# Optimization experiments

Measured on AMD Instinct MI355X. Metric: run time of the kernel, lower is better.

The kernel has to match this reference:

```python
import jax, jax.numpy as jnp
import numpy as np

B, P, D, H, DH = 2, 2048, 1024, 16, 64
EPS = 1e-5

def layernorm(x, g, b):
    mu = jnp.mean(x, axis=-1, keepdims=True)
    var = jnp.mean((x - mu) ** 2, axis=-1, keepdims=True)
    return (x - mu) * jax.lax.rsqrt(var + EPS) * g + b

def setup_inputs() -> dict:
    key = jax.random.key(0)
    ks = jax.random.split(key, 16)
    s = lambda *sh: 1.0 / np.sqrt(sh[-2] if len(sh) > 1 else sh[-1])
    return {
        "x": jax.random.normal(ks[0], (B, P, D), jnp.float32),
        "Wq": jax.random.normal(ks[1], (H, D, DH), jnp.float32) / np.sqrt(D),
        "Wk": jax.random.normal(ks[2], (H, D, DH), jnp.float32) / np.sqrt(D),
        "Wv": jax.random.normal(ks[3], (H, D, DH), jnp.float32) / np.sqrt(D),
        "Wp": jax.random.normal(ks[4], (D, D), jnp.float32) / np.sqrt(D),
        "bp": jax.random.normal(ks[5], (D,), jnp.float32) * 0.01,
        "W1": jax.random.normal(ks[6], (D, 4 * D), jnp.float32) / np.sqrt(D),
        "b1": jax.random.normal(ks[7], (4 * D,), jnp.float32) * 0.01,
        "W2": jax.random.normal(ks[8], (4 * D, D), jnp.float32) / np.sqrt(4 * D),
        "b2": jax.random.normal(ks[9], (D,), jnp.float32) * 0.01,
        "g1": jnp.ones((D,), jnp.float32),
        "be1": jnp.zeros((D,), jnp.float32),
        "g2": jnp.ones((D,), jnp.float32),
        "be2": jnp.zeros((D,), jnp.float32),
    }

def reference(x, Wq, Wk, Wv, Wp, bp, W1, b1, W2, b2, g1, be1, g2, be2):
    Bb, Pp, Dd = x.shape
    h = layernorm(x, g1, be1)
    # per-head projections, stacked: [B,H,P,DH]
    q = jnp.einsum('bpd,hde->bhpe', h, Wq)
    k = jnp.einsum('bpd,hde->bhpe', h, Wk)
    v = jnp.einsum('bpd,hde->bhpe', h, Wv)
    # NOTE: source scales by dim_embd**-0.5 (C = x.shape[-1]), not dim_head
    scores = jnp.einsum('bhpe,bhqe->bhpq', q, k) * (Dd ** -0.5)
    mask = jnp.tril(jnp.ones((Pp, Pp), bool))
    scores = jnp.where(mask, scores, -jnp.inf)
    att = jax.nn.softmax(scores, axis=-1)
    o = jnp.einsum('bhpq,bhqe->bhpe', att, v)
    # concat heads: [B,P,H*DH]
    o = o.transpose(0, 2, 1, 3).reshape(Bb, Pp, -1)
    x = x + o @ Wp + bp
    h2 = layernorm(x, g2, be2)
    m = jax.nn.gelu(h2 @ W1 + b1, approximate=False)
    x = x + m @ W2 + b2
    return x
```

## Files before the change

kernel.cpp:

```cpp
#include <hip/hip_runtime.h>
#include <hip/hip_bf16.h>
#include <stdint.h>

typedef unsigned short u16;
typedef __attribute__((ext_vector_type(4))) float f32x4;
typedef __attribute__((ext_vector_type(8))) short bf16x8;
typedef __attribute__((ext_vector_type(4))) short bf16x4;
typedef __attribute__((ext_vector_type(4))) unsigned short u16x4;

static __device__ __forceinline__ u16 f2bf(float f) {
    union { float f; unsigned u; } v; v.f = f;
    unsigned r = v.u + 0x7fffu + ((v.u >> 16) & 1u);
    return (u16)(r >> 16);
}

static __device__ __forceinline__ void gload_lds16(const u16* g, u16* l) {
    __builtin_amdgcn_global_load_lds(
        (const __attribute__((address_space(1))) void*)(uintptr_t)g,
        (__attribute__((address_space(3))) void*)(uint32_t)(uintptr_t)l,
        16, 0, 0);
}

__global__ __launch_bounds__(256) void transpose_cast_b(
    const float* __restrict__ W, u16* __restrict__ out,
    int K, int N, long in_bs, long out_bs)
{
    __shared__ float tile[32][33];
    const float* Wb = W + (size_t)blockIdx.z * in_bs;
    u16* ob = out + (size_t)blockIdx.z * out_bs;
    int nt = blockIdx.x * 32, kt = blockIdx.y * 32;
    int tx = threadIdx.x & 31, ty = threadIdx.x >> 5;
    #pragma unroll
    for (int i = ty; i < 32; i += 8)
        tile[i][tx] = Wb[(size_t)(kt + i) * N + nt + tx];
    __syncthreads();
    #pragma unroll
    for (int i = ty; i < 32; i += 8)
        ob[(size_t)(nt + i) * K + kt + tx] = f2bf(tile[tx][i]);
}

__global__ __launch_bounds__(256) void ln_kernel(
    const float* __restrict__ x, const float* __restrict__ g,
    const float* __restrict__ be, u16* __restrict__ out)
{
    int row = blockIdx.x;
    int t = threadIdx.x;
    const float4* xr = (const float4*)(x + (size_t)row * 1024);
    float4 v = xr[t];
    float s = v.x + v.y + v.z + v.w;
    float sq = v.x * v.x + v.y * v.y + v.z * v.z + v.w * v.w;
    #pragma unroll
    for (int o = 1; o < 64; o <<= 1) {
        s  += __shfl_xor(s, o);
        sq += __shfl_xor(sq, o);
    }
    __shared__ float ps[4], pq[4];
    if ((t & 63) == 0) { ps[t >> 6] = s; pq[t >> 6] = sq; }
    __syncthreads();
    float S = ps[0] + ps[1] + ps[2] + ps[3];
    float Q = pq[0] + pq[1] + pq[2] + pq[3];
    float mu = S * (1.0f / 1024.0f);
    float var = Q * (1.0f / 1024.0f) - mu * mu;
    float rs = rsqrtf(var + 1e-5f);
    const float4 g4  = ((const float4*)g)[t];
    const float4 be4 = ((const float4*)be)[t];
    u16x4 o4;
    o4[0] = f2bf((v.x - mu) * rs * g4.x + be4.x);
    o4[1] = f2bf((v.y - mu) * rs * g4.y + be4.y);
    o4[2] = f2bf((v.z - mu) * rs * g4.z + be4.z);
    o4[3] = f2bf((v.w - mu) * rs * g4.w + be4.w);
    *(u16x4*)(out + (size_t)row * 1024 + t * 4) = o4;
}

template<int EPI>
__global__ __launch_bounds__(256) void gemm_bt(
    const u16* __restrict__ A, const u16* __restrict__ Bt,
    int M, int N, int K,
    const float* __restrict__ bias,
    void* __restrict__ Cout, u16* __restrict__ Kf, u16* __restrict__ Vf)
{
    __shared__ __align__(16) u16 SH[32768];
    const int tm = blockIdx.y * 128, tn = blockIdx.x * 128;
    const int t = threadIdx.x;
    const int lane = t & 63, wave = t >> 6;
    const int wr = wave >> 1, wc = wave & 1;
    const int lq = lane & 15, lg = lane >> 4;
    f32x4 acc[4][4] = {};

    const int srow8 = lane >> 3;
    const int skoff = ((lane & 7) ^ srow8) * 8;
    const u16* ag = A  + (size_t)(tm + wave * 32 + srow8) * K + skoff;
    const u16* bg = Bt + (size_t)(tn + wave * 32 + srow8) * K + skoff;

    auto STAGE = [&](int buf, int k0) {
        u16* ab = SH + buf * 16384 + wave * 2048;
        u16* bb = SH + buf * 16384 + 8192 + wave * 2048;
        #pragma unroll
        for (int j = 0; j < 4; ++j) {
            gload_lds16(ag + (size_t)(j * 8) * K + k0, ab + j * 512);
            gload_lds16(bg + (size_t)(j * 8) * K + k0, bb + j * 512);
        }
    };

    const int KT = K >> 6;
    STAGE(0, 0);
    STAGE(1, 64);
    asm volatile("s_waitcnt vmcnt(8)" ::: "memory");
    __builtin_amdgcn_sched_barrier(0);
    __builtin_amdgcn_s_barrier();

    for (int kt = 0; kt < KT; ++kt) {
        const int buf = kt & 1;
        const u16* abuf = SH + buf * 16384;
        const u16* bbuf = abuf + 8192;
        bf16x8 af[4][2], bfv[4][2];
        #pragma unroll
        for (int m = 0; m < 4; ++m) {
            const int row = wr * 64 + m * 16 + lq;
            #pragma unroll
            for (int kk = 0; kk < 2; ++kk) {
                const int slot = (kk * 4 + lg) ^ (row & 7);
                af[m][kk] = *(const bf16x8*)(abuf + row * 64 + slot * 8);
            }
        }
        #pragma unroll
        for (int n = 0; n < 4; ++n) {
            const int col = wc * 64 + n * 16 + lq;
            #pragma unroll
            for (int kk = 0; kk < 2; ++kk) {
                const int slot = (kk * 4 + lg) ^ (col & 7);
                bfv[n][kk] = *(const bf16x8*)(bbuf + col * 64 + slot * 8);
            }
        }
        asm volatile("s_waitcnt lgkmcnt(0)" ::: "memory");
        __builtin_amdgcn_sched_barrier(0);
        __builtin_amdgcn_s_barrier();

        const bool pre = (kt + 2 < KT);
        if (pre) STAGE(buf, (kt + 2) << 6);

        __builtin_amdgcn_s_setprio(1);
        #pragma unroll
        for (int m = 0; m < 4; ++m)
            #pragma unroll
            for (int n = 0; n < 4; ++n)
                #pragma unroll
                for (int kk = 0; kk < 2; ++kk)
                    acc[m][n] = __builtin_amdgcn_mfma_f32_16x16x32_bf16(
                        af[m][kk], bfv[n][kk], acc[m][n], 0, 0, 0);
        __builtin_amdgcn_s_setprio(0);

        if (kt + 1 < KT) {
            if (pre) asm volatile("s_waitcnt vmcnt(8)" ::: "memory");
            else     asm volatile("s_waitcnt vmcnt(0)" ::: "memory");
            __builtin_amdgcn_sched_barrier(0);
            __builtin_amdgcn_s_barrier();
        }
    }

    if (EPI == 2 || (EPI == 3 && tn < 1024)) {
        __syncthreads();
        #pragma unroll
        for (int n = 0; n < 4; ++n) {
            const int cl = wc * 64 + n * 16 + lq;
            #pragma unroll
            for (int m = 0; m < 4; ++m) {
                const int rl = wr * 64 + m * 16 + lg * 4;
                #pragma unroll
                for (int r = 0; r < 4; ++r) {
                    float v = acc[m][n][r];
                    if (EPI == 2) {
                        float xx = v + bias[tn + cl];
                        v = 0.5f * xx * (1.0f + erff(xx * 0.70710678118654752f));
                    }
                    SH[(rl + r) * 136 + cl] = f2bf(v);
                }
            }
        }
        __syncthreads();
        const int row = t >> 1, half = t & 1;
        const int ncols = (EPI == 2) ? N : 1024;
        const uint4* srow4 = (const uint4*)(SH + row * 136 + half * 64);
        uint4* drow = (uint4*)((u16*)Cout + (size_t)(tm + row) * ncols + tn + half * 64);
        #pragma unroll
        for (int i = 0; i < 8; ++i)
            drow[i] = srow4[i];
    } else if (EPI == 3) {
        __syncthreads();
        const bool isK = (tn < 2048);
        #pragma unroll
        for (int n = 0; n < 4; ++n) {
            const int cl = wc * 64 + n * 16 + lq;
            const int d = cl & 63, hl = cl >> 6;
            #pragma unroll
            for (int m = 0; m < 4; ++m) {
                const int rl0 = wr * 64 + m * 16 + lg * 4;
                #pragma unroll
                for (int r = 0; r < 4; ++r) {
                    const int rl = rl0 + r;
                    const int p = rl & 63, kl = rl >> 6;
                    int off;
                    if (isK)
                        off = ((p >> 4) * 2 + (d >> 5)) * 512 + ((d >> 3) & 3) * 128
                            + (p & 15) * 8 + (d & 7);
                    else
                        off = ((p >> 4) * 4 + (d >> 4)) * 256 + ((p >> 2) & 3) * 64
                            + (d & 15) * 4 + (p & 3);
                    SH[(hl * 2 + kl) * 4096 + off] = f2bf(acc[m][n][r]);
                }
            }
        }
        __syncthreads();
        const int img = t >> 6, ln = t & 63;
        const int hl = img >> 1, kl = img & 1;
        const int hh = ((tn - (isK ? 1024 : 2048)) >> 6) + hl;
        const int bb = tm >> 11, pp = tm & 2047;
        u16* base = (isK ? Kf : Vf) + (size_t)(bb * 16 + hh) * 131072
                  + (size_t)((pp >> 6) + kl) * 4096;
        const u16* simg = SH + img * 4096;
        #pragma unroll
        for (int i = 0; i < 8; ++i)
            *(uint4*)(base + ln * 8 + i * 512) = *(const uint4*)(simg + ln * 8 + i * 512);
    }
}

__global__ __launch_bounds__(256) void gemm_bt64(
    const u16* __restrict__ A, const u16* __restrict__ Bt,
    int M, int N, int K,
    const float* __restrict__ bias, const float* __restrict__ res,
    float* __restrict__ Cout)
{
    __shared__ __align__(16) u16 SH[24576];
    const int tm = blockIdx.y * 128, tn = blockIdx.x * 64;
    const int t = threadIdx.x;
    const int lane = t & 63, wave = t >> 6;
    const int wr = wave >> 1, wc = wave & 1;
    const int lq = lane & 15, lg = lane >> 4;
    f32x4 acc[4][2] = {};

    const int srow8 = lane >> 3;
    const int skoff = ((lane & 7) ^ srow8) * 8;
    const u16* ag = A  + (size_t)(tm + wave * 32 + srow8) * K + skoff;
    const u16* bg = Bt + (size_t)(tn + wave * 16 + srow8) * K + skoff;

    auto STAGE = [&](int buf, int k0) {
        u16* ab = SH + buf * 12288 + wave * 2048;
        u16* bb = SH + buf * 12288 + 8192 + wave * 1024;
        #pragma unroll
        for (int j = 0; j < 4; ++j)
            gload_lds16(ag + (size_t)(j * 8) * K + k0, ab + j * 512);
        #pragma unroll
        for (int j = 0; j < 2; ++j)
            gload_lds16(bg + (size_t)(j * 8) * K + k0, bb + j * 512);
    };

    const int KT = K >> 6;
    STAGE(0, 0);
    STAGE(1, 64);
    asm volatile("s_waitcnt vmcnt(6)" ::: "memory");
    __builtin_amdgcn_sched_barrier(0);
    __builtin_amdgcn_s_barrier();

    for (int kt = 0; kt < KT; ++kt) {
        const int buf = kt & 1;
        const u16* abuf = SH + buf * 12288;
        const u16* bbuf = abuf + 8192;
        bf16x8 af[4][2], bfr[2][2];
        #pragma unroll
        for (int m = 0; m < 4; ++m) {
            const int row = wr * 64 + m * 16 + lq;
            #pragma unroll
            for (int kk = 0; kk < 2; ++kk) {
                const int slot = (kk * 4 + lg) ^ (row & 7);
                af[m][kk] = *(const bf16x8*)(abuf + row * 64 + slot * 8);
            }
        }
        #pragma unroll
        for (int n = 0; n < 2; ++n) {
            const int col = wc * 32 + n * 16 + lq;
            #pragma unroll
            for (int kk = 0; kk < 2; ++kk) {
                const int slot = (kk * 4 + lg) ^ (col & 7);
                bfr[n][kk] = *(const bf16x8*)(bbuf + col * 64 + slot * 8);
            }
        }
        asm volatile("s_waitcnt lgkmcnt(0)" ::: "memory");
        __builtin_amdgcn_sched_barrier(0);
        __builtin_amdgcn_s_barrier();

        const bool pre = (kt + 2 < KT);
        if (pre) STAGE(buf, (kt + 2) << 6);

        __builtin_amdgcn_s_setprio(1);
        #pragma unroll
        for (int m = 0; m < 4; ++m)
            #pragma unroll
            for (int n = 0; n < 2; ++n)
                #pragma unroll
                for (int kk = 0; kk < 2; ++kk)
                    acc[m][n] = __builtin_amdgcn_mfma_f32_16x16x32_bf16(
                        af[m][kk], bfr[n][kk], acc[m][n], 0, 0, 0);
        __builtin_amdgcn_s_setprio(0);

        if (kt + 1 < KT) {
            if (pre) asm volatile("s_waitcnt vmcnt(6)" ::: "memory");
            else     asm volatile("s_waitcnt vmcnt(0)" ::: "memory");
            __builtin_amdgcn_sched_barrier(0);
            __builtin_amdgcn_s_barrier();
        }
    }

    #pragma unroll
    for (int m = 0; m < 4; ++m)
        #pragma unroll
        for (int n = 0; n < 2; ++n) {
            const int col = tn + wc * 32 + n * 16 + lq;
            #pragma unroll
            for (int r = 0; r < 4; ++r) {
                const int row = tm + wr * 64 + m * 16 + lg * 4 + r;
                Cout[(size_t)row * N + col] = acc[m][n][r] + bias[col] + res[(size_t)row * N + col];
            }
        }
}

__global__ __launch_bounds__(256, 4) void attn_kernel(
    const u16* __restrict__ qb, const u16* __restrict__ Kf,
    const u16* __restrict__ Vf, u16* __restrict__ o)
{
    const int P = 2048;
    __shared__ __align__(16) u16 KB[2][4096];
    __shared__ __align__(16) u16 VB[2][4096];
    int blk = blockIdx.x;
    int qt = 31 - (blk >> 5);
    int bh = blk & 31;
    int h = bh & 15, b = bh >> 4;
    int w = threadIdx.x >> 6, lane = threadIdx.x & 63;
    int lq = lane & 15, lg = lane >> 4;
    int q0 = qt * 64 + w * 16;
    const u16* qptr = qb + (size_t)(b * P + q0 + lq) * 1024 + h * 64 + lg * 8;
    bf16x8 qf0 = *(const bf16x8*)qptr;
    bf16x8 qf1 = *(const bf16x8*)(qptr + 32);
    const u16* Kfb = Kf + (size_t)bh * 131072;
    const u16* Vfb = Vf + (size_t)bh * 131072;
    const float C2 = 0.03125f * 1.44269504f;
    const int moff = w * 16 + lq;
    float m2 = -1e30f, l_run = 0.f;
    f32x4 accO[4] = {};
    const int nkvb = qt + 1;

    const int vsel = w >> 1, half = w & 1;
    auto STAGE = [&](int buf, int kvb) {
        const u16* src = (vsel ? Vfb : Kfb) + (size_t)kvb * 4096 + half * 2048 + lane * 8;
        u16* dst = (vsel ? &VB[buf][half * 2048] : &KB[buf][half * 2048]);
        #pragma unroll
        for (int i = 0; i < 4; ++i)
            gload_lds16(src + i * 512, dst + i * 512);
    };

    auto COMPUTE = [&](int buf, bool last) {
        const u16* kbase = KB[buf] + lane * 8;
        f32x4 st[4];
        #pragma unroll
        for (int ss = 0; ss < 4; ++ss) {
            bf16x8 kf0 = *(const bf16x8*)(kbase + ss * 1024);
            bf16x8 kf1 = *(const bf16x8*)(kbase + ss * 1024 + 512);
            f32x4 z = {0.f, 0.f, 0.f, 0.f};
            st[ss] = __builtin_amdgcn_mfma_f32_16x16x32_bf16(kf0, qf0, z, 0, 0, 0);
            st[ss] = __builtin_amdgcn_mfma_f32_16x16x32_bf16(kf1, qf1, st[ss], 0, 0, 0);
        }
        float rmax = -1e30f;
        #pragma unroll
        for (int ss = 0; ss < 4; ++ss)
            #pragma unroll
            for (int r = 0; r < 4; ++r) {
                float v = st[ss][r] * C2;
                if (last && (ss * 16 + lg * 4 + r > moff)) v = -1e30f;
                st[ss][r] = v;
                rmax = fmaxf(rmax, v);
            }
        rmax = fmaxf(rmax, __shfl_xor(rmax, 16));
        rmax = fmaxf(rmax, __shfl_xor(rmax, 32));
        if (__any(rmax > m2 + 11.5f)) {
            float m2n = fmaxf(m2, rmax);
            float alpha = exp2f(m2 - m2n);
            l_run *= alpha;
            #pragma unroll
            for (int r = 0; r < 4; ++r) {
                float ar = __shfl(alpha, lg * 4 + r);
                accO[0][r] *= ar; accO[1][r] *= ar; accO[2][r] *= ar; accO[3][r] *= ar;
            }
            m2 = m2n;
        }
        float psum = 0.f;
        bf16x4 pf[4];
        #pragma unroll
        for (int ss = 0; ss < 4; ++ss)
            #pragma unroll
            for (int r = 0; r < 4; ++r) {
                float pv = exp2f(st[ss][r] - m2);
                psum += pv;
                pf[ss][r] = (short)f2bf(pv);
            }
        psum += __shfl_xor(psum, 16);
        psum += __shfl_xor(psum, 32);
        l_run += psum;
        const u16* vbase = VB[buf] + lane * 4;
        #pragma unroll
        for (int ks = 0; ks < 4; ++ks)
            #pragma unroll
            for (int c = 0; c < 4; ++c) {
                bf16x4 vfr = *(const bf16x4*)(vbase + (ks * 4 + c) * 256);
                accO[c] = __builtin_amdgcn_mfma_f32_16x16x16bf16_1k(pf[ks], vfr, accO[c], 0, 0, 0);
            }
    };

    STAGE(0, 0);
    __syncthreads();
    int cur = 0;
    for (int kvb = 0; kvb < nkvb; ++kvb) {
        if (kvb + 1 < nkvb) STAGE(cur ^ 1, kvb + 1);
        COMPUTE(cur, kvb == nkvb - 1);
        __syncthreads();
        cur ^= 1;
    }

    #pragma unroll
    for (int r = 0; r < 4; ++r) {
        float l_r = __shfl(l_run, lg * 4 + r);
        float inv = 1.0f / l_r;
        size_t orow = (size_t)(b * P + q0 + lg * 4 + r) * 1024 + h * 64;
        #pragma unroll
        for (int c = 0; c < 4; ++c)
            o[orow + c * 16 + lq] = f2bf(accO[c][r] * inv);
    }
}

extern "C" void kernel_launch(void* const* d_in, const int* in_sizes, int n_in,
                              void* d_out, int out_size, void* d_ws, size_t ws_size,
                              hipStream_t stream)
{
    const float* x   = (const float*)d_in[0];
    const float* Wq  = (const float*)d_in[1];
    const float* Wk  = (const float*)d_in[2];
    const float* Wv  = (const float*)d_in[3];
    const float* Wp  = (const float*)d_in[4];
    const float* bp  = (const float*)d_in[5];
    const float* W1  = (const float*)d_in[6];
    const float* b1  = (const float*)d_in[7];
    const float* W2  = (const float*)d_in[8];
    const float* b2  = (const float*)d_in[9];
    const float* g1  = (const float*)d_in[10];
    const float* be1 = (const float*)d_in[11];
    const float* g2  = (const float*)d_in[12];
    const float* be2 = (const float*)d_in[13];

    char* ws = (char*)d_ws;
    u16*  h     = (u16*)(ws + 0);
    u16*  qbuf  = (u16*)(ws + 8388608);
    u16*  Kf    = (u16*)(ws + 16777216);
    u16*  Vf    = (u16*)(ws + 25165824);
    u16*  o     = (u16*)(ws + 33554432);
    float* x1   = (float*)(ws + 41943040);
    u16*  wqkvT = (u16*)(ws + 58720256);
    u16*  wpT   = (u16*)(ws + 65011712);
    u16*  w1T   = (u16*)(ws + 67108864);
    u16*  w2T   = (u16*)(ws + 75497472);
    u16*  m     = (u16*)(ws + 0);
    u16*  h2    = o;
    float* out  = (float*)d_out;

    transpose_cast_b<<<dim3(2, 32, 16), 256, 0, stream>>>(Wq, wqkvT,           1024, 64, 65536, 65536);
    transpose_cast_b<<<dim3(2, 32, 16), 256, 0, stream>>>(Wk, wqkvT + 1048576, 1024, 64, 65536, 65536);
    transpose_cast_b<<<dim3(2, 32, 16), 256, 0, stream>>>(Wv, wqkvT + 2097152, 1024, 64, 65536, 65536);
    transpose_cast_b<<<dim3(32, 32, 1), 256, 0, stream>>>(Wp, wpT, 1024, 1024, 0, 0);
    transpose_cast_b<<<dim3(128, 32, 1), 256, 0, stream>>>(W1, w1T, 1024, 4096, 0, 0);
    transpose_cast_b<<<dim3(32, 128, 1), 256, 0, stream>>>(W2, w2T, 4096, 1024, 0, 0);

    ln_kernel<<<4096, 256, 0, stream>>>(x, g1, be1, h);
    gemm_bt<3><<<dim3(24, 32), 256, 0, stream>>>(h, wqkvT, 4096, 3072, 1024, nullptr, qbuf, Kf, Vf);
    attn_kernel<<<1024, 256, 0, stream>>>(qbuf, Kf, Vf, o);
    gemm_bt64<<<dim3(16, 32), 256, 0, stream>>>(o, wpT, 4096, 1024, 1024, bp, x, x1);
    ln_kernel<<<4096, 256, 0, stream>>>(x1, g2, be2, h2);
    gemm_bt<2><<<dim3(32, 32), 256, 0, stream>>>(h2, w1T, 4096, 4096, 1024, b1, m, nullptr, nullptr);
    gemm_bt64<<<dim3(16, 32), 256, 0, stream>>>(m, w2T, 4096, 1024, 4096, b2, x1, out);
}
```

Before: 239.3 us.

## Add 256x256 tile, 1024-thread GEMM kernel for the MLP up-projection

Replaces the W1 GEMM (previously gemm_bt<2> on a 32x32 grid of smaller tiles) with a new kernel that uses 256x256 output tiles, 16 waves per block, double-buffered direct-to-LDS loads with an XOR swizzle, and raised wave priority around the MFMA block. The bias and exact-erf GELU epilogue is staged through LDS in four row chunks so the bf16 stores to global memory are coalesced. The larger tile raises arithmetic intensity and cuts global traffic per FLOP. In exchange there are only 256 blocks, which is about one block per CU, so there is little latency hiding across blocks. The per-k-step barriers across 1024 threads may also stall.

```diff
diff --git a/kernel.cpp b/kernel.cpp
--- a/kernel.cpp
+++ b/kernel.cpp
@@ -221,6 +221,104 @@
         #pragma unroll
         for (int i = 0; i < 8; ++i)
             *(uint4*)(base + ln * 8 + i * 512) = *(const uint4*)(simg + ln * 8 + i * 512);
+    }
+}
+
+__global__ __launch_bounds__(1024, 4) void gemm256m(
+    const u16* __restrict__ A, const u16* __restrict__ Bt,
+    int M, int N, int K,
+    const float* __restrict__ bias, u16* __restrict__ Cout)
+{
+    __shared__ __align__(16) u16 SH[32768];
+    const int tm = blockIdx.y * 256, tn = blockIdx.x * 256;
+    const int t = threadIdx.x;
+    const int lane = t & 63, w = t >> 6;
+    const int wm = w >> 2, wn = w & 3;
+    const int lq = lane & 15, lg = lane >> 4;
+    f32x4 acc[4][4] = {};
+
+    const int srow = lane >> 2;
+    const int sslot = ((lane & 3) ^ ((srow >> 1) & 3)) * 8;
+    const u16* ag = A  + (size_t)(tm + w * 16 + srow) * K + sslot;
+    const u16* bg = Bt + (size_t)(tn + w * 16 + srow) * K + sslot;
+
+    auto STAGE = [&](int buf, int k0) {
+        gload_lds16(ag + k0, SH + buf * 16384 + w * 512);
+        gload_lds16(bg + k0, SH + buf * 16384 + 8192 + w * 512);
+    };
+
+    const int KT = K >> 5;
+    STAGE(0, 0);
+    STAGE(1, 32);
+    asm volatile("s_waitcnt vmcnt(2)" ::: "memory");
+    __builtin_amdgcn_sched_barrier(0);
+    __builtin_amdgcn_s_barrier();
+
+    for (int kt = 0; kt < KT; ++kt) {
+        const int buf = kt & 1;
+        const u16* abuf = SH + buf * 16384;
+        const u16* bbuf = abuf + 8192;
+        bf16x8 af[4], bfv[4];
+        #pragma unroll
+        for (int m = 0; m < 4; ++m) {
+            const int row = wm * 64 + m * 16 + lq;
+            af[m] = *(const bf16x8*)(abuf + row * 32 + (lg ^ ((row >> 1) & 3)) * 8);
+        }
+        #pragma unroll
+        for (int n = 0; n < 4; ++n) {
+            const int col = wn * 64 + n * 16 + lq;
+            bfv[n] = *(const bf16x8*)(bbuf + col * 32 + (lg ^ ((col >> 1) & 3)) * 8);
+        }
+        asm volatile("s_waitcnt lgkmcnt(0)" ::: "memory");
+        __builtin_amdgcn_sched_barrier(0);
+        __builtin_amdgcn_s_barrier();
+
+        const bool pre = (kt + 2 < KT);
+        if (pre) STAGE(buf, (kt + 2) << 5);
+
+        __builtin_amdgcn_s_setprio(1);
+        #pragma unroll
+        for (int m = 0; m < 4; ++m)
+            #pragma unroll
+            for (int n = 0; n < 4; ++n)
+                acc[m][n] = __builtin_amdgcn_mfma_f32_16x16x32_bf16(
+                    af[m], bfv[n], acc[m][n], 0, 0, 0);
+        __builtin_amdgcn_s_setprio(0);
+
+        if (kt + 1 < KT) {
+            if (pre) asm volatile("s_waitcnt vmcnt(2)" ::: "memory");
+            else     asm volatile("s_waitcnt vmcnt(0)" ::: "memory");
+            __builtin_amdgcn_sched_barrier(0);
+            __builtin_amdgcn_s_barrier();
+        }
+    }
+
+    __syncthreads();
+    #pragma unroll
+    for (int rh = 0; rh < 4; ++rh) {
+        if (rh) __syncthreads();
+        if (wm == rh) {
+            #pragma unroll
+            for (int n = 0; n < 4; ++n) {
+                const int cl = wn * 64 + n * 16 + lq;
+                #pragma unroll
+                for (int m = 0; m < 4; ++m) {
+                    const int rl = m * 16 + lg * 4;
+                    #pragma unroll
+                    for (int r = 0; r < 4; ++r) {
+                        float xx = acc[m][n][r] + bias[tn + cl];
+                        float ge = 0.5f * xx * (1.0f + erff(xx * 0.70710678118654752f));
+                        SH[(rl + r) * 264 + cl] = f2bf(ge);
+                    }
+                }
+            }
+        }
+        __syncthreads();
+        const int row = t >> 4, q = t & 15;
+        const u16* src = SH + row * 264 + q * 16;
+        u16* dst = Cout + (size_t)(tm + rh * 64 + row) * N + tn + q * 16;
+        *(uint4*)dst       = *(const uint4*)src;
+        *(uint4*)(dst + 8) = *(const uint4*)(src + 8);
     }
 }
 
@@ -481,6 +579,6 @@
     attn_kernel<<<1024, 256, 0, stream>>>(qbuf, Kf, Vf, o);
     gemm_bt64<<<dim3(16, 32), 256, 0, stream>>>(o, wpT, 4096, 1024, 1024, bp, x, x1);
     ln_kernel<<<4096, 256, 0, stream>>>(x1, g2, be2, h2);
-    gemm_bt<2><<<dim3(32, 32), 256, 0, stream>>>(h2, w1T, 4096, 4096, 1024, b1, m, nullptr, nullptr);
+    gemm256m<<<dim3(16, 16), 1024, 0, stream>>>(h2, w1T, 4096, 4096, 1024, b1, m);
     gemm_bt64<<<dim3(16, 32), 256, 0, stream>>>(m, w2T, 4096, 1024, 4096, b2, x1, out);
 }
```

Result: slower. 378.7 us (+58.3%).
